# Optimization experiments

Hardware: AMD Instinct MI355X
Metric: run time of the kernel (lower is better)

Reference implementation:

```python
import jax, jax.numpy as jnp
import numpy as np

# Eigenvalue spec: (alpha, omega, multiplicity); field='complex' => d_state = sum(mul)
EIGS = [(-0.4, 0.0, 32), (-0.3, 3.14, 32), (-0.2, 6.28, 32), (-0.1, 12.57, 32),
        (-0.05, 25.13, 32), (-0.02, 50.27, 32), (-0.01, 100.53, 32), (-0.005, 201.06, 32)]
DELTA_MIN, DELTA_MAX = 1e-3, 1e-1
B_SZ, H, L = 8, 128, 8192  # batch, d_input, seq length


def setup_inputs() -> dict:
    key = jax.random.key(0)
    k_delta, k_bre, k_bim, k_cre, k_cim, k_d, k_u = jax.random.split(key, 7)
    # continuous-time diagonal state matrix Lambda (P,) complex
    Lam = np.concatenate([np.full(m, a + 1j * w, dtype=np.complex64) for a, w, m in EIGS])
    Lambda = jnp.asarray(Lam)  # (P,)
    P = Lambda.shape[0]
    # ZOH discretization (done at init in the torch module)
    Delta = DELTA_MIN + (DELTA_MAX - DELTA_MIN) * jax.random.uniform(k_delta, (P,), dtype=jnp.float32)
    Lambda_bar = jnp.exp(Lambda * Delta)  # (P,) complex64
    B = (jax.random.normal(k_bre, (P, H), dtype=jnp.float32)
         + 1j * jax.random.normal(k_bim, (P, H), dtype=jnp.float32))
    B_bar = (((Lambda_bar - 1.0) / Lambda)[:, None] * B).astype(jnp.complex64)  # (P,H)
    C_re = jax.random.normal(k_cre, (H, P), dtype=jnp.float32)
    C_im = jax.random.normal(k_cim, (H, P), dtype=jnp.float32)
    D = jax.random.normal(k_d, (H, H), dtype=jnp.float32)
    u = jax.random.normal(k_u, (B_SZ, H, L), dtype=jnp.float32)
    return {
        "u": u,
        "Lambda_bar_re": jnp.real(Lambda_bar), "Lambda_bar_im": jnp.imag(Lambda_bar),
        "B_bar_re": jnp.real(B_bar), "B_bar_im": jnp.imag(B_bar),
        "C_re": C_re, "C_im": C_im, "D": D,
    }


def reference(u, Lambda_bar_re, Lambda_bar_im, B_bar_re, B_bar_im, C_re, C_im, D):
    Lambda_bar = Lambda_bar_re + 1j * Lambda_bar_im          # (P,)
    B_bar = B_bar_re + 1j * B_bar_im                         # (P,H)
    C = C_re + 1j * C_im                                     # (H,P)
    uc = u.astype(B_bar.dtype)
    Bu = jnp.einsum('ph,bhl->bpl', B_bar, uc)                # (B,P,L) complex
    A = jnp.broadcast_to(Lambda_bar[None, :, None], Bu.shape)  # (B,P,L)
    # The repo's binary op computes the sequential recurrence x_t = A_t * (x_{t-1} + Bu_t).
    # Rewriting with Bu'_t = A_t * Bu_t gives x_t = A_t x_{t-1} + Bu'_t, which is the
    # standard (truly associative) first-order scan.
    ABu = A * Bu

    def binop(ei, ej):
        a_i, b_i = ei
        a_j, b_j = ej
        return a_j * a_i, a_j * b_i + b_j

    _, xs = jax.lax.associative_scan(binop, (A, ABu), axis=2)  # xs: (B,P,L)
    y = jnp.einsum('op,bpl->bol', C, xs).real + jnp.einsum('oh,bhl->bol', D, u)
    return jax.nn.gelu(y, approximate=False)  # torch nn.GELU default = exact erf
```

## Files before the change

kernel.cpp:

```cpp
#include <hip/hip_runtime.h>
#include <math.h>

#define Bn 8
#define Hd 128
#define Ld 8192
#define Pd 256
#define LC 32
#define NC 256

typedef __attribute__((ext_vector_type(8))) short bf16x8;
typedef __attribute__((ext_vector_type(4))) float f32x4;
#define MFMA16(a, b, c) __builtin_amdgcn_mfma_f32_16x16x32_bf16(a, b, c, 0, 0, 0)

__device__ __forceinline__ unsigned short f2bf(float f) {
  unsigned u = __float_as_uint(f);
  u = u + 0x7fffu + ((u >> 16) & 1u);
  return (unsigned short)(u >> 16);
}

#if __has_builtin(__builtin_amdgcn_cvt_pk_bf16_f32)
typedef __attribute__((ext_vector_type(2))) __bf16 v2bf_t;
__device__ __forceinline__ unsigned pack2(float a, float b) {
  v2bf_t r = __builtin_amdgcn_cvt_pk_bf16_f32(a, b);
  unsigned u;
  __builtin_memcpy(&u, &r, 4);
  return u;
}
#else
__device__ __forceinline__ unsigned pack2(float a, float b) {
  return (unsigned)f2bf(a) | ((unsigned)f2bf(b) << 16);
}
#endif

__device__ __forceinline__ float bflo(unsigned v) { return __uint_as_float(v << 16); }
__device__ __forceinline__ float bfhi(unsigned v) { return __uint_as_float(v & 0xffff0000u); }

__device__ __forceinline__ int bperm(int p) {
  return ((p & 4) << 2) | ((p & 16) >> 1) | ((p & 8) >> 1) | (p & 3);
}

__global__ void k_prep(const float* __restrict__ Bre, const float* __restrict__ Bim,
                       const float* __restrict__ Cre, const float* __restrict__ Cim,
                       const float* __restrict__ Dm,
                       bf16x8* __restrict__ Bfr, bf16x8* __restrict__ Bfi,
                       bf16x8* __restrict__ Cf, bf16x8* __restrict__ Df) {
  int tid = blockIdx.x * 256 + threadIdx.x;
  int lane = tid & 63, slot = tid >> 6;
  int q = lane >> 4, ln = lane & 15;
  if (slot < 64) {
    int ks = slot >> 4, mt = slot & 15;
    int p = mt * 16 + ln;
    bf16x8 vr, vi;
#pragma unroll
    for (int e = 0; e < 8; ++e) {
      int h = ks * 32 + q * 8 + e;
      vr[e] = (short)f2bf(Bre[p * Hd + h]);
      vi[e] = (short)f2bf(Bim[p * Hd + h]);
    }
    Bfr[slot * 64 + lane] = vr;
    Bfi[slot * 64 + lane] = vi;
  } else if (slot < 64 + 128) {
    int s2 = slot - 64;
    int ks = s2 >> 3, mt = s2 & 7;
    int o = mt * 16 + ln;
    bf16x8 v;
#pragma unroll
    for (int e = 0; e < 8; ++e) {
      int kp = ks * 32 + q * 8 + e;
      int p = kp >> 1;
      float val = (kp & 1) ? -Cim[o * Pd + p] : Cre[o * Pd + p];
      v[e] = (short)f2bf(val);
    }
    Cf[s2 * 64 + lane] = v;
  } else if (slot < 64 + 128 + 32) {
    int s3 = slot - 192;
    int ks = s3 >> 3, mt = s3 & 7;
    int o = mt * 16 + ln;
    bf16x8 v;
#pragma unroll
    for (int e = 0; e < 8; ++e) {
      int h = ks * 32 + q * 8 + e;
      v[e] = (short)f2bf(Dm[o * Hd + h]);
    }
    Df[s3 * 64 + lane] = v;
  }
}

__device__ __forceinline__ void stage_u(const float* __restrict__ ub, unsigned* us32, int t) {
  int lane = t & 63, w = t >> 6;
  int j0 = 4 * (lane & 7);
  int h2 = 16 * w + 2 * (lane >> 3);
  const float* r0 = ub + (size_t)h2 * Ld + j0;
  float4 a0 = *(const float4*)r0;
  float4 a1 = *(const float4*)(r0 + Ld);
  const float* r2 = r0 + (size_t)64 * Ld;
  float4 b0 = *(const float4*)r2;
  float4 b1 = *(const float4*)(r2 + Ld);
  float ta0[4] = {a0.x, a0.y, a0.z, a0.w};
  float ta1[4] = {a1.x, a1.y, a1.z, a1.w};
  float tb0[4] = {b0.x, b0.y, b0.z, b0.w};
  float tb1[4] = {b1.x, b1.y, b1.z, b1.w};
#pragma unroll
  for (int i = 0; i < 4; ++i) {
    int j = j0 + i;
    int g1 = (h2 >> 3) ^ (j & 7);
    us32[(j * 256 + (g1 << 4) + ((2 * h2) & 15)) >> 2] = pack2(ta0[i], ta1[i]);
    int hb = h2 + 64;
    int g2 = (hb >> 3) ^ (j & 7);
    us32[(j * 256 + (g2 << 4) + ((2 * hb) & 15)) >> 2] = pack2(tb0[i], tb1[i]);
  }
}

__device__ __forceinline__ void compute_bu(const unsigned* us32,
                                           const bf16x8* __restrict__ Bfr,
                                           const bf16x8* __restrict__ Bfi,
                                           unsigned* bu32, int t) {
  int lane = t & 63, w = t >> 6, q = lane >> 4, ln = lane & 15;
  f32x4 zz = {0.f, 0.f, 0.f, 0.f};
  f32x4 aR[4][2], aI[4][2];
#pragma unroll
  for (int mt = 0; mt < 4; ++mt)
#pragma unroll
    for (int n = 0; n < 2; ++n) { aR[mt][n] = zz; aI[mt][n] = zz; }

#pragma unroll
  for (int ks = 0; ks < 4; ++ks) {
    bf16x8 ubf[2];
#pragma unroll
    for (int n = 0; n < 2; ++n) {
      int j = 16 * n + ln;
      int g = (4 * ks + q) ^ (j & 7);
      ubf[n] = *(const bf16x8*)((const char*)us32 + j * 256 + g * 16);
    }
#pragma unroll
    for (int mt = 0; mt < 4; ++mt) {
      int tI = ks * 16 + w * 4 + mt;
      bf16x8 ar = Bfr[tI * 64 + lane];
      bf16x8 ai = Bfi[tI * 64 + lane];
#pragma unroll
      for (int n = 0; n < 2; ++n) {
        aR[mt][n] = MFMA16(ar, ubf[n], aR[mt][n]);
        aI[mt][n] = MFMA16(ai, ubf[n], aI[mt][n]);
      }
    }
  }
#pragma unroll
  for (int mt = 0; mt < 4; ++mt)
#pragma unroll
    for (int n = 0; n < 2; ++n)
#pragma unroll
      for (int r = 0; r < 4; ++r) {
        int p = w * 64 + mt * 16 + q * 4 + r;
        int j = 16 * n + ln;
        bu32[(p << 5) | (j ^ bperm(p))] = pack2(aR[mt][n][r], aI[mt][n][r]);
      }
}

__global__ __launch_bounds__(256, 4) void k_chunk(
    const float* __restrict__ u, const float* __restrict__ lre,
    const float* __restrict__ lim, const bf16x8* __restrict__ Bfr,
    const bf16x8* __restrict__ Bfi, float2* __restrict__ E) {
  int bc = blockIdx.x;
  int b = bc >> 8, c = bc & 255;
  __shared__ __align__(16) unsigned char smem[8192 + 32768];
  unsigned* us32 = (unsigned*)smem;
  unsigned* bu32 = (unsigned*)(smem + 8192);
  int t = threadIdx.x;

  stage_u(u + (size_t)b * Hd * Ld + c * LC, us32, t);
  __syncthreads();
  compute_bu(us32, Bfr, Bfi, bu32, t);
  __syncthreads();

  int p = t;
  int pm = bperm(p);
  float ax = lre[p], ay = lim[p];
  float xr = 0.f, xi = 0.f;
#pragma unroll
  for (int j = 0; j < LC; ++j) {
    unsigned v = bu32[(p << 5) | (j ^ pm)];
    float sr = xr + bflo(v), si = xi + bfhi(v);
    xr = ax * sr - ay * si;
    xi = ax * si + ay * sr;
  }
  E[(size_t)bc * Pd + p] = make_float2(xr, xi);
}

__global__ __launch_bounds__(256) void k_scan(const float* __restrict__ lre,
                                              const float* __restrict__ lim,
                                              float2* __restrict__ E) {
  int g = blockIdx.x * 256 + threadIdx.x;
  int b = g >> 11;
  int p = (g >> 3) & 255;
  int rq = g & 7;
  float ax = lre[p], ay = lim[p];
  float sx = ax, sy = ay;
#pragma unroll
  for (int k = 0; k < 5; ++k) {
    float nx = sx * sx - sy * sy, ny = 2.f * sx * sy;
    sx = nx; sy = ny;
  }
  size_t base = ((size_t)(b * NC + rq * 32)) * Pd + p;
  float2 pre[32];
  float cr = 0.f, ci = 0.f;
#pragma unroll 8
  for (int i = 0; i < 32; ++i) {
    float2 e = E[base + (size_t)i * Pd];
    pre[i] = make_float2(cr, ci);
    float nx = sx * cr - sy * ci + e.x;
    float ny = sx * ci + sy * cr + e.y;
    cr = nx; ci = ny;
  }
  float Sx = sx, Sy = sy;
#pragma unroll
  for (int k = 0; k < 5; ++k) {
    float nx = Sx * Sx - Sy * Sy, ny = 2.f * Sx * Sy;
    Sx = nx; Sy = ny;
  }
  float Vx = cr, Vy = ci;
  float Mx = Sx, My = Sy;
#pragma unroll
  for (int d = 1; d < 8; d <<= 1) {
    float ux = __shfl_up(Vx, d, 8);
    float uy = __shfl_up(Vy, d, 8);
    if (rq >= d) {
      Vx += Mx * ux - My * uy;
      Vy += Mx * uy + My * ux;
    }
    float nx = Mx * Mx - My * My, ny = 2.f * Mx * My;
    Mx = nx; My = ny;
  }
  float Cx = __shfl_up(Vx, 1, 8);
  float Cy = __shfl_up(Vy, 1, 8);
  if (rq == 0) { Cx = 0.f; Cy = 0.f; }
  float tx = 1.f, ty = 0.f;
#pragma unroll 8
  for (int i = 0; i < 32; ++i) {
    float ox = pre[i].x + tx * Cx - ty * Cy;
    float oy = pre[i].y + tx * Cy + ty * Cx;
    E[base + (size_t)i * Pd] = make_float2(ox, oy);
    float nx = tx * sx - ty * sy, ny = tx * sy + ty * sx;
    tx = nx; ty = ny;
  }
}

__global__ __launch_bounds__(256, 4) void k_main(
    const float* __restrict__ u, const float* __restrict__ lre,
    const float* __restrict__ lim, const bf16x8* __restrict__ Bfr,
    const bf16x8* __restrict__ Bfi, const bf16x8* __restrict__ Cf,
    const bf16x8* __restrict__ Df, const float2* __restrict__ E,
    float* __restrict__ out) {
  int bc = blockIdx.x;
  int b = bc >> 8, c = bc & 255;
  __shared__ __align__(16) unsigned char smem[8192 + 32768];
  unsigned* us32 = (unsigned*)smem;
  unsigned* bu32 = (unsigned*)(smem + 8192);
  unsigned* xs32 = bu32;
  int t = threadIdx.x;
  int lane = t & 63, w = t >> 6, q = lane >> 4, ln = lane & 15;

  stage_u(u + (size_t)b * Hd * Ld + c * LC, us32, t);
  __syncthreads();
  compute_bu(us32, Bfr, Bfi, bu32, t);
  __syncthreads();

  int p = t;
  int pm = bperm(p);
  unsigned v[LC];
#pragma unroll
  for (int j = 0; j < LC; ++j) v[j] = bu32[(p << 5) | (j ^ pm)];
  float2 xin = E[(size_t)bc * Pd + p];
  __syncthreads();

  {
    float ax = lre[p], ay = lim[p];
    float xr = xin.x, xi = xin.y;
#pragma unroll
    for (int j = 0; j < LC; ++j) {
      float sr = xr + bflo(v[j]), si = xi + bfhi(v[j]);
      xr = ax * sr - ay * si;
      xi = ax * si + ay * sr;
      xs32[j * 256 + ((((p >> 2) ^ (j & 7)) << 2) + (p & 3))] = pack2(xr, xi);
    }
  }
  __syncthreads();

  f32x4 zz = {0.f, 0.f, 0.f, 0.f};
  f32x4 acc[2][2] = {{zz, zz}, {zz, zz}};
#pragma unroll
  for (int ks = 0; ks < 16; ++ks) {
    bf16x8 xb[2];
#pragma unroll
    for (int n = 0; n < 2; ++n) {
      int j = 16 * n + ln;
      int g = (4 * ks + q) ^ (j & 7);
      xb[n] = *(const bf16x8*)((const char*)xs32 + j * 1024 + g * 16);
    }
#pragma unroll
    for (int mt = 0; mt < 2; ++mt) {
      bf16x8 cf = Cf[(ks * 8 + w * 2 + mt) * 64 + lane];
#pragma unroll
      for (int n = 0; n < 2; ++n) acc[mt][n] = MFMA16(cf, xb[n], acc[mt][n]);
    }
  }
#pragma unroll
  for (int ks = 0; ks < 4; ++ks) {
    bf16x8 ubf[2];
#pragma unroll
    for (int n = 0; n < 2; ++n) {
      int j = 16 * n + ln;
      int g = (4 * ks + q) ^ (j & 7);
      ubf[n] = *(const bf16x8*)((const char*)us32 + j * 256 + g * 16);
    }
#pragma unroll
    for (int mt = 0; mt < 2; ++mt) {
      bf16x8 df = Df[(ks * 8 + w * 2 + mt) * 64 + lane];
#pragma unroll
      for (int n = 0; n < 2; ++n) acc[mt][n] = MFMA16(df, ubf[n], acc[mt][n]);
    }
  }

#pragma unroll
  for (int mt = 0; mt < 2; ++mt)
#pragma unroll
    for (int n = 0; n < 2; ++n)
#pragma unroll
      for (int r = 0; r < 4; ++r) {
        int o = w * 32 + mt * 16 + q * 4 + r;
        int l = c * LC + 16 * n + ln;
        float vy = acc[mt][n][r];
        float e2 = __builtin_amdgcn_exp2f(-2.4554670f * vy);
        float gy = vy * __builtin_amdgcn_rcpf(1.0f + e2);
        out[((size_t)(b * Hd + o)) * Ld + l] = gy;
      }
}

extern "C" void kernel_launch(void* const* d_in, const int* in_sizes, int n_in,
                              void* d_out, int out_size, void* d_ws, size_t ws_size,
                              hipStream_t stream) {
  const float* u   = (const float*)d_in[0];
  const float* lre = (const float*)d_in[1];
  const float* lim = (const float*)d_in[2];
  const float* Bre = (const float*)d_in[3];
  const float* Bim = (const float*)d_in[4];
  const float* Cre = (const float*)d_in[5];
  const float* Cim = (const float*)d_in[6];
  const float* Dm  = (const float*)d_in[7];
  float* out = (float*)d_out;

  char* ws = (char*)d_ws;
  bf16x8* Bfr = (bf16x8*)(ws);
  bf16x8* Bfi = (bf16x8*)(ws + 65536);
  bf16x8* Cf  = (bf16x8*)(ws + 131072);
  bf16x8* Df  = (bf16x8*)(ws + 262144);
  float2* E   = (float2*)(ws + (1 << 20));

  k_prep<<<56, 256, 0, stream>>>(Bre, Bim, Cre, Cim, Dm, Bfr, Bfi, Cf, Df);
  k_chunk<<<Bn * NC, 256, 0, stream>>>(u, lre, lim, Bfr, Bfi, E);
  k_scan<<<64, 256, 0, stream>>>(lre, lim, E);
  k_main<<<Bn * NC, 256, 0, stream>>>(u, lre, lim, Bfr, Bfi, Cf, Df, E, out);
}
```

Before: 153.0 us.

## Store Bu and D·u from chunk pass to global, skip recompute in main pass

The chunk kernel now also computes the D·u product and writes both the packed Bu values and the D·u partial outputs to workspace buffers. The main kernel reads these back instead of restaging u and recomputing Bu and D·u with MFMAs, and its occupancy hint is raised. This removes duplicated matrix work and the shared-memory staging of u in the main pass. In exchange it adds roughly 80 MB of extra global writes and reads per call.

```diff
diff --git a/kernel.cpp b/kernel.cpp
--- a/kernel.cpp
+++ b/kernel.cpp
@@ -111,79 +111,102 @@
   }
 }
 
-__device__ __forceinline__ void compute_bu(const unsigned* us32,
-                                           const bf16x8* __restrict__ Bfr,
-                                           const bf16x8* __restrict__ Bfi,
-                                           unsigned* bu32, int t) {
-  int lane = t & 63, w = t >> 6, q = lane >> 4, ln = lane & 15;
-  f32x4 zz = {0.f, 0.f, 0.f, 0.f};
-  f32x4 aR[4][2], aI[4][2];
-#pragma unroll
-  for (int mt = 0; mt < 4; ++mt)
-#pragma unroll
-    for (int n = 0; n < 2; ++n) { aR[mt][n] = zz; aI[mt][n] = zz; }
-
-#pragma unroll
-  for (int ks = 0; ks < 4; ++ks) {
-    bf16x8 ubf[2];
-#pragma unroll
-    for (int n = 0; n < 2; ++n) {
-      int j = 16 * n + ln;
-      int g = (4 * ks + q) ^ (j & 7);
-      ubf[n] = *(const bf16x8*)((const char*)us32 + j * 256 + g * 16);
-    }
-#pragma unroll
-    for (int mt = 0; mt < 4; ++mt) {
-      int tI = ks * 16 + w * 4 + mt;
-      bf16x8 ar = Bfr[tI * 64 + lane];
-      bf16x8 ai = Bfi[tI * 64 + lane];
-#pragma unroll
-      for (int n = 0; n < 2; ++n) {
-        aR[mt][n] = MFMA16(ar, ubf[n], aR[mt][n]);
-        aI[mt][n] = MFMA16(ai, ubf[n], aI[mt][n]);
-      }
-    }
-  }
-#pragma unroll
-  for (int mt = 0; mt < 4; ++mt)
-#pragma unroll
-    for (int n = 0; n < 2; ++n)
-#pragma unroll
-      for (int r = 0; r < 4; ++r) {
-        int p = w * 64 + mt * 16 + q * 4 + r;
-        int j = 16 * n + ln;
-        bu32[(p << 5) | (j ^ bperm(p))] = pack2(aR[mt][n][r], aI[mt][n][r]);
-      }
-}
-
 __global__ __launch_bounds__(256, 4) void k_chunk(
     const float* __restrict__ u, const float* __restrict__ lre,
     const float* __restrict__ lim, const bf16x8* __restrict__ Bfr,
-    const bf16x8* __restrict__ Bfi, float2* __restrict__ E) {
+    const bf16x8* __restrict__ Bfi, const bf16x8* __restrict__ Df,
+    float2* __restrict__ E, unsigned* __restrict__ bu_g,
+    unsigned* __restrict__ du_g) {
   int bc = blockIdx.x;
   int b = bc >> 8, c = bc & 255;
   __shared__ __align__(16) unsigned char smem[8192 + 32768];
   unsigned* us32 = (unsigned*)smem;
   unsigned* bu32 = (unsigned*)(smem + 8192);
   int t = threadIdx.x;
+  int lane = t & 63, w = t >> 6, q = lane >> 4, ln = lane & 15;
 
   stage_u(u + (size_t)b * Hd * Ld + c * LC, us32, t);
   __syncthreads();
-  compute_bu(us32, Bfr, Bfi, bu32, t);
+
+  f32x4 zz = {0.f, 0.f, 0.f, 0.f};
+  f32x4 aR[4][2], aI[4][2], dA[2][2];
+#pragma unroll
+  for (int mt = 0; mt < 4; ++mt)
+#pragma unroll
+    for (int n = 0; n < 2; ++n) { aR[mt][n] = zz; aI[mt][n] = zz; }
+#pragma unroll
+  for (int mt = 0; mt < 2; ++mt)
+#pragma unroll
+    for (int n = 0; n < 2; ++n) dA[mt][n] = zz;
+
+#pragma unroll
+  for (int ks = 0; ks < 4; ++ks) {
+    bf16x8 ubf[2];
+#pragma unroll
+    for (int n = 0; n < 2; ++n) {
+      int j = 16 * n + ln;
+      int g = (4 * ks + q) ^ (j & 7);
+      ubf[n] = *(const bf16x8*)((const char*)us32 + j * 256 + g * 16);
+    }
+#pragma unroll
+    for (int mt = 0; mt < 4; ++mt) {
+      int tI = ks * 16 + w * 4 + mt;
+      bf16x8 ar = Bfr[tI * 64 + lane];
+      bf16x8 ai = Bfi[tI * 64 + lane];
+#pragma unroll
+      for (int n = 0; n < 2; ++n) {
+        aR[mt][n] = MFMA16(ar, ubf[n], aR[mt][n]);
+        aI[mt][n] = MFMA16(ai, ubf[n], aI[mt][n]);
+      }
+    }
+#pragma unroll
+    for (int mt = 0; mt < 2; ++mt) {
+      bf16x8 df = Df[(ks * 8 + w * 2 + mt) * 64 + lane];
+#pragma unroll
+      for (int n = 0; n < 2; ++n) dA[mt][n] = MFMA16(df, ubf[n], dA[mt][n]);
+    }
+  }
+
+#pragma unroll
+  for (int mt = 0; mt < 2; ++mt)
+#pragma unroll
+    for (int r = 0; r < 4; ++r) {
+      int o = w * 32 + mt * 16 + q * 4 + r;
+      du_g[(size_t)bc * 2048 + o * 16 + ln] = pack2(dA[mt][0][r], dA[mt][1][r]);
+    }
+
+#pragma unroll
+  for (int mt = 0; mt < 4; ++mt)
+#pragma unroll
+    for (int n = 0; n < 2; ++n)
+#pragma unroll
+      for (int r = 0; r < 4; ++r) {
+        int p = w * 64 + mt * 16 + q * 4 + r;
+        int j = 16 * n + ln;
+        bu32[(p << 5) | (j ^ bperm(p))] = pack2(aR[mt][n][r], aI[mt][n][r]);
+      }
   __syncthreads();
 
   int p = t;
   int pm = bperm(p);
+  unsigned v[LC];
+#pragma unroll
+  for (int j = 0; j < LC; ++j) v[j] = bu32[(p << 5) | (j ^ pm)];
+
   float ax = lre[p], ay = lim[p];
   float xr = 0.f, xi = 0.f;
 #pragma unroll
   for (int j = 0; j < LC; ++j) {
-    unsigned v = bu32[(p << 5) | (j ^ pm)];
-    float sr = xr + bflo(v), si = xi + bfhi(v);
+    float sr = xr + bflo(v[j]), si = xi + bfhi(v[j]);
     xr = ax * sr - ay * si;
     xi = ax * si + ay * sr;
   }
   E[(size_t)bc * Pd + p] = make_float2(xr, xi);
+
+  uint4* dst = (uint4*)(bu_g + ((size_t)bc << 13) + (p << 5));
+#pragma unroll
+  for (int i = 0; i < 8; ++i)
+    dst[i] = make_uint4(v[4 * i], v[4 * i + 1], v[4 * i + 2], v[4 * i + 3]);
 }
 
 __global__ __launch_bounds__(256) void k_scan(const float* __restrict__ lre,
@@ -244,34 +267,26 @@
   }
 }
 
-__global__ __launch_bounds__(256, 4) void k_main(
-    const float* __restrict__ u, const float* __restrict__ lre,
-    const float* __restrict__ lim, const bf16x8* __restrict__ Bfr,
-    const bf16x8* __restrict__ Bfi, const bf16x8* __restrict__ Cf,
-    const bf16x8* __restrict__ Df, const float2* __restrict__ E,
+__global__ __launch_bounds__(256, 5) void k_main(
+    const float* __restrict__ lre, const float* __restrict__ lim,
+    const bf16x8* __restrict__ Cf, const float2* __restrict__ E,
+    const unsigned* __restrict__ bu_g, const unsigned* __restrict__ du_g,
     float* __restrict__ out) {
   int bc = blockIdx.x;
   int b = bc >> 8, c = bc & 255;
-  __shared__ __align__(16) unsigned char smem[8192 + 32768];
-  unsigned* us32 = (unsigned*)smem;
-  unsigned* bu32 = (unsigned*)(smem + 8192);
-  unsigned* xs32 = bu32;
+  __shared__ __align__(16) unsigned xs32[LC * 256];
   int t = threadIdx.x;
   int lane = t & 63, w = t >> 6, q = lane >> 4, ln = lane & 15;
 
-  stage_u(u + (size_t)b * Hd * Ld + c * LC, us32, t);
-  __syncthreads();
-  compute_bu(us32, Bfr, Bfi, bu32, t);
-  __syncthreads();
-
   int p = t;
-  int pm = bperm(p);
   unsigned v[LC];
-#pragma unroll
-  for (int j = 0; j < LC; ++j) v[j] = bu32[(p << 5) | (j ^ pm)];
+  const uint4* src = (const uint4*)(bu_g + ((size_t)bc << 13) + (p << 5));
+#pragma unroll
+  for (int i = 0; i < 8; ++i) {
+    uint4 x = src[i];
+    v[4 * i] = x.x; v[4 * i + 1] = x.y; v[4 * i + 2] = x.z; v[4 * i + 3] = x.w;
+  }
   float2 xin = E[(size_t)bc * Pd + p];
-  __syncthreads();
-
   {
     float ax = lre[p], ay = lim[p];
     float xr = xin.x, xi = xin.y;
@@ -303,36 +318,24 @@
       for (int n = 0; n < 2; ++n) acc[mt][n] = MFMA16(cf, xb[n], acc[mt][n]);
     }
   }
-#pragma unroll
-  for (int ks = 0; ks < 4; ++ks) {
-    bf16x8 ubf[2];
-#pragma unroll
-    for (int n = 0; n < 2; ++n) {
-      int j = 16 * n + ln;
-      int g = (4 * ks + q) ^ (j & 7);
-      ubf[n] = *(const bf16x8*)((const char*)us32 + j * 256 + g * 16);
-    }
-#pragma unroll
-    for (int mt = 0; mt < 2; ++mt) {
-      bf16x8 df = Df[(ks * 8 + w * 2 + mt) * 64 + lane];
-#pragma unroll
-      for (int n = 0; n < 2; ++n) acc[mt][n] = MFMA16(df, ubf[n], acc[mt][n]);
-    }
-  }
 
 #pragma unroll
   for (int mt = 0; mt < 2; ++mt)
 #pragma unroll
-    for (int n = 0; n < 2; ++n)
-#pragma unroll
-      for (int r = 0; r < 4; ++r) {
-        int o = w * 32 + mt * 16 + q * 4 + r;
+    for (int r = 0; r < 4; ++r) {
+      int o = w * 32 + mt * 16 + q * 4 + r;
+      unsigned d32 = du_g[(size_t)bc * 2048 + o * 16 + ln];
+      acc[mt][0][r] += bflo(d32);
+      acc[mt][1][r] += bfhi(d32);
+#pragma unroll
+      for (int n = 0; n < 2; ++n) {
         int l = c * LC + 16 * n + ln;
         float vy = acc[mt][n][r];
         float e2 = __builtin_amdgcn_exp2f(-2.4554670f * vy);
         float gy = vy * __builtin_amdgcn_rcpf(1.0f + e2);
         out[((size_t)(b * Hd + o)) * Ld + l] = gy;
       }
+    }
 }
 
 extern "C" void kernel_launch(void* const* d_in, const int* in_sizes, int n_in,
@@ -349,14 +352,16 @@
   float* out = (float*)d_out;
 
   char* ws = (char*)d_ws;
-  bf16x8* Bfr = (bf16x8*)(ws);
-  bf16x8* Bfi = (bf16x8*)(ws + 65536);
-  bf16x8* Cf  = (bf16x8*)(ws + 131072);
-  bf16x8* Df  = (bf16x8*)(ws + 262144);
-  float2* E   = (float2*)(ws + (1 << 20));
+  bf16x8*  Bfr  = (bf16x8*)(ws);
+  bf16x8*  Bfi  = (bf16x8*)(ws + 65536);
+  bf16x8*  Cf   = (bf16x8*)(ws + 131072);
+  bf16x8*  Df   = (bf16x8*)(ws + 262144);
+  float2*  E    = (float2*)(ws + (1 << 20));
+  unsigned* bu_g = (unsigned*)(ws + (8ull << 20));
+  unsigned* du_g = (unsigned*)(ws + (80ull << 20));
 
   k_prep<<<56, 256, 0, stream>>>(Bre, Bim, Cre, Cim, Dm, Bfr, Bfi, Cf, Df);
-  k_chunk<<<Bn * NC, 256, 0, stream>>>(u, lre, lim, Bfr, Bfi, E);
+  k_chunk<<<Bn * NC, 256, 0, stream>>>(u, lre, lim, Bfr, Bfi, Df, E, bu_g, du_g);
   k_scan<<<64, 256, 0, stream>>>(lre, lim, E);
-  k_main<<<Bn * NC, 256, 0, stream>>>(u, lre, lim, Bfr, Bfi, Cf, Df, E, out);
-}
+  k_main<<<Bn * NC, 256, 0, stream>>>(lre, lim, Cf, E, bu_g, du_g, out);
+}
```

Result: slower. 165.1 us (+7.9%).
